# Kernel optimization log

Hardware: AMD Instinct MI355X
Metric: run time of the kernel (lower is better)

## Reference

```python
import jax, jax.numpy as jnp
import numpy as np

SEQ_LEN = 2048

def setup_inputs() -> dict:
    key = jax.random.key(0)
    kq, kk, kv = jax.random.split(key, 3)
    B, S, D = 8, SEQ_LEN, 64
    q = jax.random.normal(kq, (B, S, D), dtype=jnp.float32)
    k = jax.random.normal(kk, (B, S, D), dtype=jnp.float32)
    v = jax.random.normal(kv, (B, S, D), dtype=jnp.float32)
    return {"q": q, "k": k, "v": v}

def reference(q, k, v):
    # scores: [B, S, S] = q @ k^T  (note: original applies NO 1/sqrt(d) scaling)
    scores = jnp.einsum('bqd,bkd->bqk', q, k)
    S = scores.shape[-1]
    causal = jnp.tril(jnp.ones((S, S), dtype=bool))  # lower-triangular mask
    scores = jnp.where(causal, scores, -jnp.inf)
    weights = jax.nn.softmax(scores, axis=-1)
    return jnp.einsum('bqk,bkd->bqd', weights, v)
```

## Files before the change

### kernel.cpp

```cpp
#include <hip/hip_runtime.h>


#define BATCH 8
#define SEQ 2048
#define DIM 64
#define NEL (BATCH * SEQ * DIM)

typedef __attribute__((ext_vector_type(8))) short short8;
typedef __attribute__((ext_vector_type(4))) float f32x4;

#define MFMA(a, b, c) __builtin_amdgcn_mfma_f32_16x16x32_bf16(a, b, c, 0, 0, 0)

__device__ __forceinline__ unsigned short f2bf(float x) {
    unsigned u = __float_as_uint(x);
    unsigned r = u + 0x7fffu + ((u >> 16) & 1u);
    return (unsigned short)(r >> 16);
}
__device__ __forceinline__ float bf2f(unsigned short h) {
    return __uint_as_float(((unsigned)h) << 16);
}
__device__ __forceinline__ short8 ld8(const unsigned short* p) {
    return *(const short8*)p;
}
__device__ __forceinline__ void splitA(float4 a, float4 b, short8& h8, short8& l8) {
    float v[8] = {a.x, a.y, a.z, a.w, b.x, b.y, b.z, b.w};
#pragma unroll
    for (int i = 0; i < 8; ++i) {
        unsigned u  = __float_as_uint(v[i]);
        unsigned hu = u & 0xffff0000u;
        h8[i] = (short)(hu >> 16);
        float lf = v[i] - __uint_as_float(hu);
        l8[i] = (short)(__float_as_uint(lf) >> 16);
    }
}

__device__ __forceinline__ float dpp_max16(float x) {
    float o;
    o = __int_as_float(__builtin_amdgcn_update_dpp(0, __float_as_int(x), 0xB1, 0xF, 0xF, true));
    x = fmaxf(x, o);
    o = __int_as_float(__builtin_amdgcn_update_dpp(0, __float_as_int(x), 0x4E, 0xF, 0xF, true));
    x = fmaxf(x, o);
    o = __int_as_float(__builtin_amdgcn_update_dpp(0, __float_as_int(x), 0x141, 0xF, 0xF, true));
    x = fmaxf(x, o);
    o = __int_as_float(__builtin_amdgcn_update_dpp(0, __float_as_int(x), 0x140, 0xF, 0xF, true));
    return fmaxf(x, o);
}
__device__ __forceinline__ float dpp_sum16(float x) {
    float o;
    o = __int_as_float(__builtin_amdgcn_update_dpp(0, __float_as_int(x), 0xB1, 0xF, 0xF, true));
    x += o;
    o = __int_as_float(__builtin_amdgcn_update_dpp(0, __float_as_int(x), 0x4E, 0xF, 0xF, true));
    x += o;
    o = __int_as_float(__builtin_amdgcn_update_dpp(0, __float_as_int(x), 0x141, 0xF, 0xF, true));
    x += o;
    o = __int_as_float(__builtin_amdgcn_update_dpp(0, __float_as_int(x), 0x140, 0xF, 0xF, true));
    return x + o;
}

__global__ __launch_bounds__(256) void prep(
    const float* __restrict__ K, const float* __restrict__ V,
    unsigned short* __restrict__ Kh, unsigned short* __restrict__ Kl,
    unsigned short* __restrict__ Vf)
{
    __shared__ unsigned short sT[64][72];
    const int blk = blockIdx.x;
    const int t = threadIdx.x;

    if (blk < 1024) {
        const int off = (blk * 256 + t) * 4;
        float4 v = *(const float4*)(K + off);
        ushort4 h, l;
        h.x = f2bf(v.x); l.x = f2bf(v.x - bf2f(h.x));
        h.y = f2bf(v.y); l.y = f2bf(v.y - bf2f(h.y));
        h.z = f2bf(v.z); l.z = f2bf(v.z - bf2f(h.z));
        h.w = f2bf(v.w); l.w = f2bf(v.w - bf2f(h.w));
        *(ushort4*)(Kh + off) = h;
        *(ushort4*)(Kl + off) = l;
        return;
    }

    const int tile = blk - 1024;
    const int b = tile >> 5;
    const int s0 = (tile & 31) * 64;
    const int srow = t >> 4;
    const int d4   = (t & 15) * 4;
#pragma unroll
    for (int i = 0; i < 4; ++i) {
        const int row = srow + i * 16;
        float4 v = *(const float4*)(V + ((size_t)(b * SEQ + s0 + row)) * DIM + d4);
        sT[d4 + 0][row] = f2bf(v.x);
        sT[d4 + 1][row] = f2bf(v.y);
        sT[d4 + 2][row] = f2bf(v.z);
        sT[d4 + 3][row] = f2bf(v.w);
    }
    __syncthreads();
#pragma unroll
    for (int i = 0; i < 2; ++i) {
        const int fid = t + i * 256;
        const int cc  = fid >> 8;
        const int nt  = (fid >> 6) & 3;
        const int l   = fid & 63;
        const int key = cc * 32 + (l >> 4) * 8;
        const int dim = nt * 16 + (l & 15);
        const int c   = (s0 >> 5) + cc;
        unsigned short* dst =
            Vf + ((((size_t)(b * 64 + c)) * 4 + nt) << 9) + l * 8;
        *(float4*)dst = *(const float4*)&sT[dim][key];
    }
}

__global__ __launch_bounds__(256) void attn_main(
    const float* __restrict__ Q,
    const unsigned short* __restrict__ Kh, const unsigned short* __restrict__ Kl,
    const unsigned short* __restrict__ Vf, float* __restrict__ O)
{
    __shared__ __align__(16) char scratch[4][4352];
    __shared__ float sMl[4][16][2];

    const int bid  = blockIdx.x;
    const int b    = bid & (BATCH - 1);
    const int pair = bid >> 3;

    const int t    = threadIdx.x;
    const int w    = t >> 6;
    const int lane = t & 63;
    const int quad = lane >> 4;
    const int n16  = lane & 15;
    const int boff = b * SEQ;

    unsigned short* sPw = (unsigned short*)scratch[w];
    float*          sOw = (float*)scratch[w];

    for (int half = 0; half < 2; ++half) {
        const int qt = half ? (127 - pair) : pair;
        const int q0 = qt * 16;
        const int q_max = q0 + 15;

        short8 qh0, ql0, qh1, ql1;
        {
            const float* qb = Q + ((size_t)(boff + q0 + n16)) * DIM + quad * 8;
            splitA(*(const float4*)(qb),      *(const float4*)(qb + 4),  qh0, ql0);
            splitA(*(const float4*)(qb + 32), *(const float4*)(qb + 36), qh1, ql1);
        }

        float m0 = -1e30f, m1 = -1e30f, m2 = -1e30f, m3 = -1e30f;
        float l0 = 0.f, l1 = 0.f, l2 = 0.f, l3 = 0.f;
        f32x4 oacc[4];
#pragma unroll
        for (int i = 0; i < 4; ++i) oacc[i] = (f32x4){0.f, 0.f, 0.f, 0.f};

        for (int kb = w * 128; kb <= q_max; kb += 512) {
            const int rem  = q_max - kb;
            const int nsub = min(8, (rem >> 4) + 1);
            const int nchain = (nsub + 1) >> 1;
            f32x4 sacc[8];

#pragma unroll
            for (int gp = 0; gp < 4; ++gp) {
                const int stA = 2 * gp, stB = stA + 1;
                if (stA < nsub) {
                    const size_t krA = (size_t)(boff + kb + stA * 16 + n16) * DIM + quad * 8;
                    short8 khA0 = ld8(Kh + krA), khA1 = ld8(Kh + krA + 32);
                    short8 klA0 = ld8(Kl + krA), klA1 = ld8(Kl + krA + 32);
                    const bool okB = (stB < nsub);
                    const size_t krB = (size_t)(boff + kb + stB * 16 + n16) * DIM + quad * 8;
                    short8 khB0, khB1, klB0, klB1;
                    if (okB) {
                        khB0 = ld8(Kh + krB); khB1 = ld8(Kh + krB + 32);
                        klB0 = ld8(Kl + krB); klB1 = ld8(Kl + krB + 32);
                    }
                    f32x4 accA = (f32x4){0.f, 0.f, 0.f, 0.f};
                    accA = MFMA(qh0, khA0, accA);
                    accA = MFMA(qh1, khA1, accA);
                    accA = MFMA(qh0, klA0, accA);
                    accA = MFMA(qh1, klA1, accA);
                    accA = MFMA(ql0, khA0, accA);
                    accA = MFMA(ql1, khA1, accA);
                    sacc[stA] = accA;
                    if (okB) {
                        f32x4 accB = (f32x4){0.f, 0.f, 0.f, 0.f};
                        accB = MFMA(qh0, khB0, accB);
                        accB = MFMA(qh1, khB1, accB);
                        accB = MFMA(qh0, klB0, accB);
                        accB = MFMA(qh1, klB1, accB);
                        accB = MFMA(ql0, khB0, accB);
                        accB = MFMA(ql1, khB1, accB);
                        sacc[stB] = accB;
                    } else {
                        sacc[stB] = (f32x4){-1e30f, -1e30f, -1e30f, -1e30f};
                    }
                } else {
                    sacc[stA] = (f32x4){-1e30f, -1e30f, -1e30f, -1e30f};
                    sacc[stB] = (f32x4){-1e30f, -1e30f, -1e30f, -1e30f};
                }
            }

            if (kb + 127 > q0) {
#pragma unroll
                for (int st = 0; st < 8; ++st) {
                    if (st < nsub) {
                        const int key = kb + st * 16 + n16;
#pragma unroll
                        for (int r = 0; r < 4; ++r)
                            if (key > q0 + quad * 4 + r) sacc[st][r] = -1e30f;
                    }
                }
            }

            float mt0 = sacc[0][0], mt1 = sacc[0][1], mt2 = sacc[0][2], mt3 = sacc[0][3];
#pragma unroll
            for (int st = 1; st < 8; ++st) {
                mt0 = fmaxf(mt0, sacc[st][0]);
                mt1 = fmaxf(mt1, sacc[st][1]);
                mt2 = fmaxf(mt2, sacc[st][2]);
                mt3 = fmaxf(mt3, sacc[st][3]);
            }
            mt0 = dpp_max16(mt0); mt1 = dpp_max16(mt1);
            mt2 = dpp_max16(mt2); mt3 = dpp_max16(mt3);
            const float mn0 = fmaxf(m0, mt0), mn1 = fmaxf(m1, mt1);
            const float mn2 = fmaxf(m2, mt2), mn3 = fmaxf(m3, mt3);
            const float a0 = __expf(m0 - mn0), a1 = __expf(m1 - mn1);
            const float a2 = __expf(m2 - mn2), a3 = __expf(m3 - mn3);
            m0 = mn0; m1 = mn1; m2 = mn2; m3 = mn3;

            float ps0 = 0.f, ps1 = 0.f, ps2 = 0.f, ps3 = 0.f;
            const int stmax = 2 * nchain;
#pragma unroll
            for (int st = 0; st < 8; ++st) {
                if (st < stmax) {
                    float p0 = 0.f, p1 = 0.f, p2 = 0.f, p3 = 0.f;
                    if (st < nsub) {
                        p0 = __expf(sacc[st][0] - mn0);
                        p1 = __expf(sacc[st][1] - mn1);
                        p2 = __expf(sacc[st][2] - mn2);
                        p3 = __expf(sacc[st][3] - mn3);
                        ps0 += p0; ps1 += p1; ps2 += p2; ps3 += p3;
                    }
                    const int col = st * 16 + n16;
                    sPw[(quad * 4 + 0) * 136 + col] = f2bf(p0);
                    sPw[(quad * 4 + 1) * 136 + col] = f2bf(p1);
                    sPw[(quad * 4 + 2) * 136 + col] = f2bf(p2);
                    sPw[(quad * 4 + 3) * 136 + col] = f2bf(p3);
                }
            }
            ps0 = dpp_sum16(ps0); ps1 = dpp_sum16(ps1);
            ps2 = dpp_sum16(ps2); ps3 = dpp_sum16(ps3);
            l0 = l0 * a0 + ps0; l1 = l1 * a1 + ps1;
            l2 = l2 * a2 + ps2; l3 = l3 * a3 + ps3;
#pragma unroll
            for (int nt = 0; nt < 4; ++nt) {
                oacc[nt][0] *= a0; oacc[nt][1] *= a1;
                oacc[nt][2] *= a2; oacc[nt][3] *= a3;
            }

#pragma unroll
            for (int ch = 0; ch < 4; ++ch) {
                if (ch < nchain) {
                    short8 pa = ld8(&sPw[n16 * 136 + ch * 32 + quad * 8]);
                    const size_t cbase =
                        (((size_t)(b * 64 + (kb >> 5) + ch)) * 4) << 9;
#pragma unroll
                    for (int nt = 0; nt < 4; ++nt) {
                        short8 vv = ld8(Vf + cbase + (nt << 9) + lane * 8);
                        oacc[nt] = MFMA(pa, vv, oacc[nt]);
                    }
                }
            }
        }

#pragma unroll
        for (int nt = 0; nt < 4; ++nt)
#pragma unroll
            for (int r = 0; r < 4; ++r)
                sOw[(quad * 4 + r) * 68 + nt * 16 + n16] = oacc[nt][r];
        if (n16 == 0) {
            sMl[w][quad * 4 + 0][0] = m0; sMl[w][quad * 4 + 0][1] = l0;
            sMl[w][quad * 4 + 1][0] = m1; sMl[w][quad * 4 + 1][1] = l1;
            sMl[w][quad * 4 + 2][0] = m2; sMl[w][quad * 4 + 2][1] = l2;
            sMl[w][quad * 4 + 3][0] = m3; sMl[w][quad * 4 + 3][1] = l3;
        }
        __syncthreads();

        const int row  = t >> 4;
        const int col4 = (t & 15) * 4;
        float M = fmaxf(fmaxf(sMl[0][row][0], sMl[1][row][0]),
                        fmaxf(sMl[2][row][0], sMl[3][row][0]));
        float L = 0.f;
        float ox = 0.f, oy = 0.f, oz = 0.f, ow = 0.f;
#pragma unroll
        for (int wv = 0; wv < 4; ++wv) {
            const float ew = __expf(sMl[wv][row][0] - M);
            L += ew * sMl[wv][row][1];
            const float* op = (const float*)scratch[wv] + row * 68 + col4;
            ox += ew * op[0]; oy += ew * op[1]; oz += ew * op[2]; ow += ew * op[3];
        }
        const float inv = 1.0f / L;
        float4 res = make_float4(ox * inv, oy * inv, oz * inv, ow * inv);
        *(float4*)(O + ((size_t)(boff + q0 + row)) * DIM + col4) = res;

        __syncthreads();
    }
}

extern "C" void kernel_launch(void* const* d_in, const int* in_sizes, int n_in,
                              void* d_out, int out_size, void* d_ws, size_t ws_size,
                              hipStream_t stream) {
    const float* q = (const float*)d_in[0];
    const float* k = (const float*)d_in[1];
    const float* v = (const float*)d_in[2];
    float* out = (float*)d_out;

    unsigned short* Kh = (unsigned short*)d_ws;
    unsigned short* Kl = Kh + NEL;
    unsigned short* Vf = Kl + NEL;

    prep<<<dim3(1024 + 256), dim3(256), 0, stream>>>(k, v, Kh, Kl, Vf);
    attn_main<<<dim3(512), dim3(256), 0, stream>>>(q, Kh, Kl, Vf, out);
}
```

Baseline: 108.8 us.

## Process both paired query tiles concurrently with 512-thread blocks

Each block previously handled its two causal-balanced query tiles one after the other with 4 waves. Now the block has 8 waves, and each group of 4 handles one tile at the same time, with doubled shared scratch and one block-wide barrier. This removes the serial half loop and the extra sync, and raises the number of waves per block. In exchange it costs more LDS per block, and the launch bound of 512 threads with min 2 blocks may constrain registers.

New measurement: 116.2 us. 1.07x slower.

```diff
diff --git a/kernel.cpp b/kernel.cpp
--- a/kernel.cpp
+++ b/kernel.cpp
@@ -109,196 +109,198 @@
     }
 }
 
-__global__ __launch_bounds__(256) void attn_main(
+__global__ __launch_bounds__(512, 2) void attn_main(
     const float* __restrict__ Q,
     const unsigned short* __restrict__ Kh, const unsigned short* __restrict__ Kl,
     const unsigned short* __restrict__ Vf, float* __restrict__ O)
 {
-    __shared__ __align__(16) char scratch[4][4352];
-    __shared__ float sMl[4][16][2];
+    __shared__ __align__(16) char scratch[8][4352];
+    __shared__ float sMl[8][16][2];
 
     const int bid  = blockIdx.x;
     const int b    = bid & (BATCH - 1);
     const int pair = bid >> 3;
 
     const int t    = threadIdx.x;
-    const int w    = t >> 6;
+    const int g    = t >> 8;
+    const int wg   = t >> 6;
+    const int wl   = wg & 3;
     const int lane = t & 63;
     const int quad = lane >> 4;
     const int n16  = lane & 15;
     const int boff = b * SEQ;
 
-    unsigned short* sPw = (unsigned short*)scratch[w];
-    float*          sOw = (float*)scratch[w];
-
-    for (int half = 0; half < 2; ++half) {
-        const int qt = half ? (127 - pair) : pair;
-        const int q0 = qt * 16;
-        const int q_max = q0 + 15;
-
-        short8 qh0, ql0, qh1, ql1;
-        {
-            const float* qb = Q + ((size_t)(boff + q0 + n16)) * DIM + quad * 8;
-            splitA(*(const float4*)(qb),      *(const float4*)(qb + 4),  qh0, ql0);
-            splitA(*(const float4*)(qb + 32), *(const float4*)(qb + 36), qh1, ql1);
-        }
-
-        float m0 = -1e30f, m1 = -1e30f, m2 = -1e30f, m3 = -1e30f;
-        float l0 = 0.f, l1 = 0.f, l2 = 0.f, l3 = 0.f;
-        f32x4 oacc[4];
-#pragma unroll
-        for (int i = 0; i < 4; ++i) oacc[i] = (f32x4){0.f, 0.f, 0.f, 0.f};
-
-        for (int kb = w * 128; kb <= q_max; kb += 512) {
-            const int rem  = q_max - kb;
-            const int nsub = min(8, (rem >> 4) + 1);
-            const int nchain = (nsub + 1) >> 1;
-            f32x4 sacc[8];
-
-#pragma unroll
-            for (int gp = 0; gp < 4; ++gp) {
-                const int stA = 2 * gp, stB = stA + 1;
-                if (stA < nsub) {
-                    const size_t krA = (size_t)(boff + kb + stA * 16 + n16) * DIM + quad * 8;
-                    short8 khA0 = ld8(Kh + krA), khA1 = ld8(Kh + krA + 32);
-                    short8 klA0 = ld8(Kl + krA), klA1 = ld8(Kl + krA + 32);
-                    const bool okB = (stB < nsub);
-                    const size_t krB = (size_t)(boff + kb + stB * 16 + n16) * DIM + quad * 8;
-                    short8 khB0, khB1, klB0, klB1;
-                    if (okB) {
-                        khB0 = ld8(Kh + krB); khB1 = ld8(Kh + krB + 32);
-                        klB0 = ld8(Kl + krB); klB1 = ld8(Kl + krB + 32);
-                    }
-                    f32x4 accA = (f32x4){0.f, 0.f, 0.f, 0.f};
-                    accA = MFMA(qh0, khA0, accA);
-                    accA = MFMA(qh1, khA1, accA);
-                    accA = MFMA(qh0, klA0, accA);
-                    accA = MFMA(qh1, klA1, accA);
-                    accA = MFMA(ql0, khA0, accA);
-                    accA = MFMA(ql1, khA1, accA);
-                    sacc[stA] = accA;
-                    if (okB) {
-                        f32x4 accB = (f32x4){0.f, 0.f, 0.f, 0.f};
-                        accB = MFMA(qh0, khB0, accB);
-                        accB = MFMA(qh1, khB1, accB);
-                        accB = MFMA(qh0, klB0, accB);
-                        accB = MFMA(qh1, klB1, accB);
-                        accB = MFMA(ql0, khB0, accB);
-                        accB = MFMA(ql1, khB1, accB);
-                        sacc[stB] = accB;
-                    } else {
-                        sacc[stB] = (f32x4){-1e30f, -1e30f, -1e30f, -1e30f};
-                    }
+    const int qt = g ? (127 - pair) : pair;
+    const int q0 = qt * 16;
+    const int q_max = q0 + 15;
+
+    unsigned short* sPw = (unsigned short*)scratch[wg];
+    float*          sOw = (float*)scratch[wg];
+
+    short8 qh0, ql0, qh1, ql1;
+    {
+        const float* qb = Q + ((size_t)(boff + q0 + n16)) * DIM + quad * 8;
+        splitA(*(const float4*)(qb),      *(const float4*)(qb + 4),  qh0, ql0);
+        splitA(*(const float4*)(qb + 32), *(const float4*)(qb + 36), qh1, ql1);
+    }
+
+    float m0 = -1e30f, m1 = -1e30f, m2 = -1e30f, m3 = -1e30f;
+    float l0 = 0.f, l1 = 0.f, l2 = 0.f, l3 = 0.f;
+    f32x4 oacc[4];
+#pragma unroll
+    for (int i = 0; i < 4; ++i) oacc[i] = (f32x4){0.f, 0.f, 0.f, 0.f};
+
+    for (int kb = wl * 128; kb <= q_max; kb += 512) {
+        const int rem  = q_max - kb;
+        const int nsub = min(8, (rem >> 4) + 1);
+        const int nchain = (nsub + 1) >> 1;
+        f32x4 sacc[8];
+
+#pragma unroll
+        for (int gp = 0; gp < 4; ++gp) {
+            const int stA = 2 * gp, stB = stA + 1;
+            if (stA < nsub) {
+                const size_t krA = (size_t)(boff + kb + stA * 16 + n16) * DIM + quad * 8;
+                short8 khA0 = ld8(Kh + krA), khA1 = ld8(Kh + krA + 32);
+                short8 klA0 = ld8(Kl + krA), klA1 = ld8(Kl + krA + 32);
+                const bool okB = (stB < nsub);
+                const size_t krB = (size_t)(boff + kb + stB * 16 + n16) * DIM + quad * 8;
+                short8 khB0, khB1, klB0, klB1;
+                if (okB) {
+                    khB0 = ld8(Kh + krB); khB1 = ld8(Kh + krB + 32);
+                    klB0 = ld8(Kl + krB); klB1 = ld8(Kl + krB + 32);
+                }
+                f32x4 accA = (f32x4){0.f, 0.f, 0.f, 0.f};
+                accA = MFMA(qh0, khA0, accA);
+                accA = MFMA(qh1, khA1, accA);
+                accA = MFMA(qh0, klA0, accA);
+                accA = MFMA(qh1, klA1, accA);
+                accA = MFMA(ql0, khA0, accA);
+                accA = MFMA(ql1, khA1, accA);
+                sacc[stA] = accA;
+                if (okB) {
+                    f32x4 accB = (f32x4){0.f, 0.f, 0.f, 0.f};
+                    accB = MFMA(qh0, khB0, accB);
+                    accB = MFMA(qh1, khB1, accB);
+                    accB = MFMA(qh0, klB0, accB);
+                    accB = MFMA(qh1, klB1, accB);
+                    accB = MFMA(ql0, khB0, accB);
+                    accB = MFMA(ql1, khB1, accB);
+                    sacc[stB] = accB;
                 } else {
-                    sacc[stA] = (f32x4){-1e30f, -1e30f, -1e30f, -1e30f};
                     sacc[stB] = (f32x4){-1e30f, -1e30f, -1e30f, -1e30f};
                 }
+            } else {
+                sacc[stA] = (f32x4){-1e30f, -1e30f, -1e30f, -1e30f};
+                sacc[stB] = (f32x4){-1e30f, -1e30f, -1e30f, -1e30f};
             }
-
-            if (kb + 127 > q0) {
-#pragma unroll
-                for (int st = 0; st < 8; ++st) {
-                    if (st < nsub) {
-                        const int key = kb + st * 16 + n16;
-#pragma unroll
-                        for (int r = 0; r < 4; ++r)
-                            if (key > q0 + quad * 4 + r) sacc[st][r] = -1e30f;
-                    }
+        }
+
+        if (kb + 127 > q0) {
+#pragma unroll
+            for (int st = 0; st < 8; ++st) {
+                if (st < nsub) {
+                    const int key = kb + st * 16 + n16;
+#pragma unroll
+                    for (int r = 0; r < 4; ++r)
+                        if (key > q0 + quad * 4 + r) sacc[st][r] = -1e30f;
                 }
             }
-
-            float mt0 = sacc[0][0], mt1 = sacc[0][1], mt2 = sacc[0][2], mt3 = sacc[0][3];
-#pragma unroll
-            for (int st = 1; st < 8; ++st) {
-                mt0 = fmaxf(mt0, sacc[st][0]);
-                mt1 = fmaxf(mt1, sacc[st][1]);
-                mt2 = fmaxf(mt2, sacc[st][2]);
-                mt3 = fmaxf(mt3, sacc[st][3]);
+        }
+
+        float mt0 = sacc[0][0], mt1 = sacc[0][1], mt2 = sacc[0][2], mt3 = sacc[0][3];
+#pragma unroll
+        for (int st = 1; st < 8; ++st) {
+            mt0 = fmaxf(mt0, sacc[st][0]);
+            mt1 = fmaxf(mt1, sacc[st][1]);
+            mt2 = fmaxf(mt2, sacc[st][2]);
+            mt3 = fmaxf(mt3, sacc[st][3]);
+        }
+        mt0 = dpp_max16(mt0); mt1 = dpp_max16(mt1);
+        mt2 = dpp_max16(mt2); mt3 = dpp_max16(mt3);
+        const float mn0 = fmaxf(m0, mt0), mn1 = fmaxf(m1, mt1);
+        const float mn2 = fmaxf(m2, mt2), mn3 = fmaxf(m3, mt3);
+        const float a0 = __expf(m0 - mn0), a1 = __expf(m1 - mn1);
+        const float a2 = __expf(m2 - mn2), a3 = __expf(m3 - mn3);
+        m0 = mn0; m1 = mn1; m2 = mn2; m3 = mn3;
+
+        float ps0 = 0.f, ps1 = 0.f, ps2 = 0.f, ps3 = 0.f;
+        const int stmax = 2 * nchain;
+#pragma unroll
+        for (int st = 0; st < 8; ++st) {
+            if (st < stmax) {
+                float p0 = 0.f, p1 = 0.f, p2 = 0.f, p3 = 0.f;
+                if (st < nsub) {
+                    p0 = __expf(sacc[st][0] - mn0);
+                    p1 = __expf(sacc[st][1] - mn1);
+                    p2 = __expf(sacc[st][2] - mn2);
+                    p3 = __expf(sacc[st][3] - mn3);
+                    ps0 += p0; ps1 += p1; ps2 += p2; ps3 += p3;
+                }
+                const int col = st * 16 + n16;
+                sPw[(quad * 4 + 0) * 136 + col] = f2bf(p0);
+                sPw[(quad * 4 + 1) * 136 + col] = f2bf(p1);
+                sPw[(quad * 4 + 2) * 136 + col] = f2bf(p2);
+                sPw[(quad * 4 + 3) * 136 + col] = f2bf(p3);
             }
-            mt0 = dpp_max16(mt0); mt1 = dpp_max16(mt1);
-            mt2 = dpp_max16(mt2); mt3 = dpp_max16(mt3);
-            const float mn0 = fmaxf(m0, mt0), mn1 = fmaxf(m1, mt1);
-            const float mn2 = fmaxf(m2, mt2), mn3 = fmaxf(m3, mt3);
-            const float a0 = __expf(m0 - mn0), a1 = __expf(m1 - mn1);
-            const float a2 = __expf(m2 - mn2), a3 = __expf(m3 - mn3);
-            m0 = mn0; m1 = mn1; m2 = mn2; m3 = mn3;
-
-            float ps0 = 0.f, ps1 = 0.f, ps2 = 0.f, ps3 = 0.f;
-            const int stmax = 2 * nchain;
-#pragma unroll
-            for (int st = 0; st < 8; ++st) {
-                if (st < stmax) {
-                    float p0 = 0.f, p1 = 0.f, p2 = 0.f, p3 = 0.f;
-                    if (st < nsub) {
-                        p0 = __expf(sacc[st][0] - mn0);
-                        p1 = __expf(sacc[st][1] - mn1);
-                        p2 = __expf(sacc[st][2] - mn2);
-                        p3 = __expf(sacc[st][3] - mn3);
-                        ps0 += p0; ps1 += p1; ps2 += p2; ps3 += p3;
-                    }
-                    const int col = st * 16 + n16;
-                    sPw[(quad * 4 + 0) * 136 + col] = f2bf(p0);
-                    sPw[(quad * 4 + 1) * 136 + col] = f2bf(p1);
-                    sPw[(quad * 4 + 2) * 136 + col] = f2bf(p2);
-                    sPw[(quad * 4 + 3) * 136 + col] = f2bf(p3);
+        }
+        ps0 = dpp_sum16(ps0); ps1 = dpp_sum16(ps1);
+        ps2 = dpp_sum16(ps2); ps3 = dpp_sum16(ps3);
+        l0 = l0 * a0 + ps0; l1 = l1 * a1 + ps1;
+        l2 = l2 * a2 + ps2; l3 = l3 * a3 + ps3;
+#pragma unroll
+        for (int nt = 0; nt < 4; ++nt) {
+            oacc[nt][0] *= a0; oacc[nt][1] *= a1;
+            oacc[nt][2] *= a2; oacc[nt][3] *= a3;
+        }
+
+#pragma unroll
+        for (int ch = 0; ch < 4; ++ch) {
+            if (ch < nchain) {
+                short8 pa = ld8(&sPw[n16 * 136 + ch * 32 + quad * 8]);
+                const size_t cbase =
+                    (((size_t)(b * 64 + (kb >> 5) + ch)) * 4) << 9;
+#pragma unroll
+                for (int nt = 0; nt < 4; ++nt) {
+                    short8 vv = ld8(Vf + cbase + (nt << 9) + lane * 8);
+                    oacc[nt] = MFMA(pa, vv, oacc[nt]);
                 }
             }
-            ps0 = dpp_sum16(ps0); ps1 = dpp_sum16(ps1);
-            ps2 = dpp_sum16(ps2); ps3 = dpp_sum16(ps3);
-            l0 = l0 * a0 + ps0; l1 = l1 * a1 + ps1;
-            l2 = l2 * a2 + ps2; l3 = l3 * a3 + ps3;
-#pragma unroll
-            for (int nt = 0; nt < 4; ++nt) {
-                oacc[nt][0] *= a0; oacc[nt][1] *= a1;
-                oacc[nt][2] *= a2; oacc[nt][3] *= a3;
-            }
-
-#pragma unroll
-            for (int ch = 0; ch < 4; ++ch) {
-                if (ch < nchain) {
-                    short8 pa = ld8(&sPw[n16 * 136 + ch * 32 + quad * 8]);
-                    const size_t cbase =
-                        (((size_t)(b * 64 + (kb >> 5) + ch)) * 4) << 9;
-#pragma unroll
-                    for (int nt = 0; nt < 4; ++nt) {
-                        short8 vv = ld8(Vf + cbase + (nt << 9) + lane * 8);
-                        oacc[nt] = MFMA(pa, vv, oacc[nt]);
-                    }
-                }
-            }
-        }
-
-#pragma unroll
-        for (int nt = 0; nt < 4; ++nt)
-#pragma unroll
-            for (int r = 0; r < 4; ++r)
-                sOw[(quad * 4 + r) * 68 + nt * 16 + n16] = oacc[nt][r];
-        if (n16 == 0) {
-            sMl[w][quad * 4 + 0][0] = m0; sMl[w][quad * 4 + 0][1] = l0;
-            sMl[w][quad * 4 + 1][0] = m1; sMl[w][quad * 4 + 1][1] = l1;
-            sMl[w][quad * 4 + 2][0] = m2; sMl[w][quad * 4 + 2][1] = l2;
-            sMl[w][quad * 4 + 3][0] = m3; sMl[w][quad * 4 + 3][1] = l3;
-        }
-        __syncthreads();
-
-        const int row  = t >> 4;
-        const int col4 = (t & 15) * 4;
-        float M = fmaxf(fmaxf(sMl[0][row][0], sMl[1][row][0]),
-                        fmaxf(sMl[2][row][0], sMl[3][row][0]));
+        }
+    }
+
+#pragma unroll
+    for (int nt = 0; nt < 4; ++nt)
+#pragma unroll
+        for (int r = 0; r < 4; ++r)
+            sOw[(quad * 4 + r) * 68 + nt * 16 + n16] = oacc[nt][r];
+    if (n16 == 0) {
+        sMl[wg][quad * 4 + 0][0] = m0; sMl[wg][quad * 4 + 0][1] = l0;
+        sMl[wg][quad * 4 + 1][0] = m1; sMl[wg][quad * 4 + 1][1] = l1;
+        sMl[wg][quad * 4 + 2][0] = m2; sMl[wg][quad * 4 + 2][1] = l2;
+        sMl[wg][quad * 4 + 3][0] = m3; sMl[wg][quad * 4 + 3][1] = l3;
+    }
+    __syncthreads();
+
+    {
+        const int tl   = t & 255;
+        const int row  = tl >> 4;
+        const int col4 = (tl & 15) * 4;
+        const int wb   = g * 4;
+        float M = fmaxf(fmaxf(sMl[wb + 0][row][0], sMl[wb + 1][row][0]),
+                        fmaxf(sMl[wb + 2][row][0], sMl[wb + 3][row][0]));
         float L = 0.f;
         float ox = 0.f, oy = 0.f, oz = 0.f, ow = 0.f;
 #pragma unroll
         for (int wv = 0; wv < 4; ++wv) {
-            const float ew = __expf(sMl[wv][row][0] - M);
-            L += ew * sMl[wv][row][1];
-            const float* op = (const float*)scratch[wv] + row * 68 + col4;
+            const float ew = __expf(sMl[wb + wv][row][0] - M);
+            L += ew * sMl[wb + wv][row][1];
+            const float* op = (const float*)scratch[wb + wv] + row * 68 + col4;
             ox += ew * op[0]; oy += ew * op[1]; oz += ew * op[2]; ow += ew * op[3];
         }
         const float inv = 1.0f / L;
         float4 res = make_float4(ox * inv, oy * inv, oz * inv, ow * inv);
         *(float4*)(O + ((size_t)(boff + q0 + row)) * DIM + col4) = res;
-
-        __syncthreads();
     }
 }
 
@@ -315,5 +317,5 @@
     unsigned short* Vf = Kl + NEL;
 
     prep<<<dim3(1024 + 256), dim3(256), 0, stream>>>(k, v, Kh, Kl, Vf);
-    attn_main<<<dim3(512), dim3(256), 0, stream>>>(q, Kh, Kl, Vf, out);
-}
+    attn_main<<<dim3(512), dim3(512), 0, stream>>>(q, Kh, Kl, Vf, out);
+}
```
